# Performance work log

Hardware: AMD Instinct MI355X
Metric: run time of the kernel (lower is better)

Reference implementation:

```python
import jax, jax.numpy as jnp
import numpy as np

SQRT2 = 1.4142135623730951
MH_C = 0.8673250705840776  # (2/sqrt(3)) * pi**(-1/4), mexican-hat normalizer


def _bn(x, eps=1e-5):
    # BatchNorm (training-mode batch stats, default affine gamma=1, beta=0)
    mu = jnp.mean(x, axis=0, keepdims=True)
    var = jnp.var(x, axis=0, keepdims=True)
    return (x - mu) / jnp.sqrt(var + eps)


def setup_inputs() -> dict:
    key = jax.random.key(0)
    ks = jax.random.split(key, 10)
    N, F, E, B, OUT = 1024, 1024, 32768, 16, 10
    H = F // 2  # 512 after Haar DWT
    x = jax.random.normal(ks[0], (N, F), dtype=jnp.float32)
    edge_index = jax.random.randint(ks[1], (2, E), 0, N, dtype=jnp.int32)
    batch = jnp.sort(jax.random.randint(ks[2], (N,), 0, B, dtype=jnp.int32))
    w_att = jax.random.normal(ks[3], (2,), dtype=jnp.float32)  # Linear(2,1,bias=False)
    wk_scale = jnp.ones((H, H), dtype=jnp.float32)
    wk_trans = jax.random.normal(ks[4], (H, H), dtype=jnp.float32) * 0.1
    wk_wav_w = jax.random.normal(ks[5], (H, H), dtype=jnp.float32) * 0.05
    wk_base_w = jax.random.normal(ks[6], (H, H), dtype=jnp.float32) * 0.05
    fc1_w = jax.random.normal(ks[7], (512, F + H), dtype=jnp.float32) * 0.02
    fc1_b = jnp.zeros((512,), dtype=jnp.float32)
    fc2_w = jax.random.normal(ks[8], (OUT, 512), dtype=jnp.float32) * 0.02
    fc2_b = jnp.zeros((OUT,), dtype=jnp.float32)
    return {"x": x, "w_att": w_att, "wk_scale": wk_scale, "wk_trans": wk_trans,
            "wk_wav_w": wk_wav_w, "wk_base_w": wk_base_w, "fc1_w": fc1_w,
            "fc1_b": fc1_b, "fc2_w": fc2_w, "fc2_b": fc2_b,
            "edge_index": edge_index, "batch": batch, "num_graphs": B}


def reference(x, w_att, wk_scale, wk_trans, wk_wav_w, wk_base_w,
              fc1_w, fc1_b, fc2_w, fc2_b, edge_index, batch, num_graphs):
    N = x.shape[0]
    # --- WaveletAttention: Haar ('db1') DWT over the feature dim ---
    xe, xo = x[:, 0::2], x[:, 1::2]
    low = (xe + xo) / SQRT2            # [N, 512]
    high = (xe - xo) / SQRT2           # [N, 512]
    scores = jax.nn.sigmoid(low * w_att[0] + high * w_att[1])
    h = scores * low + (1.0 - scores) * high
    # --- GINConv aggregation (eps=0): self + sum of neighbor features ---
    src, dst = edge_index[0], edge_index[1]
    agg = h + jax.ops.segment_sum(h[src], dst, num_segments=N)  # [N, 512]
    # --- WavKAN layer 512->512 (mexican hat) ---
    xs = (agg[:, None, :] - wk_trans) / wk_scale                # [N, 512, 512]
    xs2 = xs * xs
    mh = MH_C * (1.0 - xs2) * jnp.exp(-0.5 * xs2)
    wav = jnp.einsum('noi,oi->no', mh, wk_wav_w)                # [N, 512]
    base = jax.nn.silu(agg) @ wk_base_w.T
    conv_out = _bn(wav + base)   # WavKAN-internal BatchNorm1d
    conv_out = _bn(conv_out)     # bn1 (dropout p=0 -> identity)
    # --- skip concat + bn2 ---
    z = _bn(jnp.concatenate([x, conv_out], axis=1))             # [N, 1536]
    # --- global mean pool over graphs ---
    sums = jax.ops.segment_sum(z, batch, num_segments=num_graphs)
    cnts = jax.ops.segment_sum(jnp.ones((N,), z.dtype), batch, num_segments=num_graphs)
    pooled = sums / jnp.maximum(cnts, 1.0)[:, None]             # [B, 1536]
    # --- classifier head (eval-mode dropout = identity) ---
    h1 = jax.nn.relu(pooled @ fc1_w.T + fc1_b)
    return h1 @ fc2_w.T + fc2_b
```

## Files before the change

kernel.cpp:

```cpp
#include <hip/hip_runtime.h>
#include <math.h>

#define N_NODES 1024
#define F_DIM   1024
#define H_DIM   512
#define E_EDGES 32768
#define B_GRAPHS 16
#define OUT_DIM 10
#define FH_DIM  1536
#define EPS 1e-5f
#define MH_C_D 0.8673250705840776
#define C2_D   0.72134752044448170368
#define C2_F   ((float)C2_D)
#define CSC    0.84932180028801904272f
#define WC2F   ((float)(MH_C_D / C2_D))
#define INV_SQRT2 0.70710678118654752440f
#define ECAP 128

typedef float v2f __attribute__((ext_vector_type(2)));
typedef unsigned int u32;
typedef const __attribute__((address_space(1))) u32 gu32;
typedef __attribute__((address_space(3))) u32 lu32;

#if __has_builtin(__builtin_amdgcn_exp2f)
#define EXP2NEG(x) __builtin_amdgcn_exp2f(-(x))
#else
#define EXP2NEG(x) __expf(-0.69314718055994530942f * (x))
#endif

#define PK_FMA_BB(d, a, p) \
    asm("v_pk_fma_f32 %0, %1, %2, %2 op_sel:[0,0,1] op_sel_hi:[1,0,1]" \
        : "=v"(d) : "v"(a), "v"(p))
#define PK_MUL2(d, a, b) \
    asm("v_pk_mul_f32 %0, %1, %2" : "=v"(d) : "v"(a), "v"(b))
#define PK_WZC(d, s, k) \
    asm("v_pk_mul_f32 %0, %1, %2 op_sel:[0,0] op_sel_hi:[0,1]" \
        : "=v"(d) : "v"(s), "v"(k))
#define PK_FMA_HI_ACC(acc, s, p) \
    asm("v_pk_fma_f32 %0, %1, %2, %0 op_sel:[0,1,0] op_sel_hi:[1,1,1]" \
        : "+v"(acc) : "v"(s), "v"(p))

__global__ __launch_bounds__(256) void k_hx(const int* __restrict__ src,
                                            const int* __restrict__ dst,
                                            int* __restrict__ deg,
                                            int* __restrict__ elist,
                                            const float* __restrict__ x,
                                            float* __restrict__ xsum,
                                            float* __restrict__ xsum2,
                                            const float* __restrict__ scale,
                                            const float* __restrict__ trans,
                                            const float* __restrict__ ww,
                                            const float* __restrict__ bw,
                                            float* __restrict__ pk,
                                            const float* __restrict__ watt,
                                            float* __restrict__ h) {
    const int bid = blockIdx.x;
    const int t = threadIdx.x;
    if (bid < 2048) {
        int idx = bid * 256 + t;
        float2 p = ((const float2*)x)[idx];
        float lo = (p.x + p.y) * INV_SQRT2;
        float hi = (p.x - p.y) * INV_SQRT2;
        float tt = lo * watt[0] + hi * watt[1];
        float sc = 1.0f / (1.0f + __expf(-tt));
        h[idx] = sc * lo + (1.0f - sc) * hi;
    } else if (bid < 3072) {
        int g = (bid - 2048) * 256 + t;
        float iv = 1.0f / scale[g];
        float4 p;
        p.x = iv * CSC;
        p.y = -(trans[g] * iv * CSC);
        p.z = -(ww[g] * WC2F);
        p.w = bw[g];
        ((float4*)pk)[g] = p;
    } else if (bid < 3200) {
        int e = (bid - 3072) * 256 + t;
        int d = dst[e];
        int slot = atomicAdd(&deg[d], 1);
        elist[d * ECAP + slot] = src[e];
    } else {
        const int n0 = (bid - 3200) * 16;
        float s[4] = {}, s2[4] = {};
        for (int r = 0; r < 16; ++r) {
            #pragma unroll
            for (int ch = 0; ch < 4; ++ch) {
                float v = x[(n0 + r) * F_DIM + ch * 256 + t];
                s[ch] += v; s2[ch] += v * v;
            }
        }
        #pragma unroll
        for (int ch = 0; ch < 4; ++ch) {
            unsafeAtomicAdd(&xsum[ch * 256 + t], s[ch]);
            unsafeAtomicAdd(&xsum2[ch * 256 + t], s2[ch]);
        }
    }
}

__global__ __launch_bounds__(256) void k_gather(const float* __restrict__ h,
                                                const int* __restrict__ deg,
                                                const int* __restrict__ elist,
                                                float* __restrict__ agg) {
    int d = blockIdx.x;
    int t = threadIdx.x;
    int st = d * ECAP, dg = deg[d];
    const float2* h2 = (const float2*)h;
    float2 a = h2[d * 256 + t];
    int k = 0;
    for (; k + 4 <= dg; k += 4) {
        int s0 = elist[st + k];
        int s1 = elist[st + k + 1];
        int s2 = elist[st + k + 2];
        int s3 = elist[st + k + 3];
        float2 v0 = h2[s0 * 256 + t];
        float2 v1 = h2[s1 * 256 + t];
        float2 v2 = h2[s2 * 256 + t];
        float2 v3 = h2[s3 * 256 + t];
        a.x += (v0.x + v1.x) + (v2.x + v3.x);
        a.y += (v0.y + v1.y) + (v2.y + v3.y);
    }
    for (; k < dg; ++k) {
        int s0 = elist[st + k];
        float2 v0 = h2[s0 * 256 + t];
        a.x += v0.x; a.y += v0.y;
    }
    ((float2*)agg)[d * 256 + t] = a;
}

__global__ __launch_bounds__(256) void k_transpose(const float* __restrict__ agg,
                                                   float* __restrict__ aggT,
                                                   float* __restrict__ siluT) {
    __shared__ float tile[64 * 65];
    const int t = threadIdx.x;
    const int n0 = blockIdx.x * 64;
    const int i0 = blockIdx.y * 64;
    #pragma unroll
    for (int v = 0; v < 4; ++v) {
        int flat = v * 256 + t;
        int r = flat >> 4, c4 = flat & 15;
        float4 a = *(const float4*)&agg[(n0 + r) * H_DIM + i0 + c4 * 4];
        tile[(c4 * 4 + 0) * 65 + r] = a.x;
        tile[(c4 * 4 + 1) * 65 + r] = a.y;
        tile[(c4 * 4 + 2) * 65 + r] = a.z;
        tile[(c4 * 4 + 3) * 65 + r] = a.w;
    }
    __syncthreads();
    #pragma unroll
    for (int v = 0; v < 4; ++v) {
        int flat = v * 256 + t;
        int il = flat >> 4, c4 = flat & 15;
        float4 a;
        a.x = tile[il * 65 + c4 * 4 + 0];
        a.y = tile[il * 65 + c4 * 4 + 1];
        a.z = tile[il * 65 + c4 * 4 + 2];
        a.w = tile[il * 65 + c4 * 4 + 3];
        int g = (i0 + il) * N_NODES + n0 + c4 * 4;
        *(float4*)&aggT[g] = a;
        float4 s;
        s.x = a.x / (1.0f + __expf(-a.x));
        s.y = a.y / (1.0f + __expf(-a.y));
        s.z = a.z / (1.0f + __expf(-a.z));
        s.w = a.w / (1.0f + __expf(-a.w));
        *(float4*)&siluT[g] = s;
    }
}

#define TN 128
#define TO 32
#define KI 16
#define TOP (TO + 1)
#define ZSPLIT 8
#define ZLEN (H_DIM / ZSPLIT)
#define NSTG (ZLEN / KI)
__global__ __launch_bounds__(256) void k_wavelet(const float* __restrict__ aggT,
                                                 const float* __restrict__ siluT,
                                                 const float* __restrict__ pk,
                                                 float* __restrict__ vbp) {
    __shared__ float  sA[2][KI * TN];
    __shared__ float  sS[2][KI * TN];
    __shared__ float4 sP4[2][KI * TOP];

    const int t  = threadIdx.x;
    const int n0 = blockIdx.x * TN;
    const int o0 = blockIdx.y * TO;
    const int z0 = blockIdx.z * ZLEN;
    const int na = (t & 15) * 4;
    const int ol = (t >> 4) * 2;

    const int srow = t >> 5, scol = (t & 31) * 4;
    const int po  = t >> 4;
    const int pii = t & 15;
    const float4* pk4 = (const float4*)pk;

    v2f accw[2][4] = {};
    v2f accb[2][4] = {};
    v2f kC2; kC2.x = 1.0f; kC2.y = -C2_F;

    {
        int g0 = (z0 + srow) * N_NODES + n0 + scol;
        int g1 = (z0 + 8 + srow) * N_NODES + n0 + scol;
        __builtin_amdgcn_global_load_lds((gu32*)&aggT[g0],  (lu32*)&sA[0][t * 4], 16, 0, 0);
        __builtin_amdgcn_global_load_lds((gu32*)&aggT[g1],  (lu32*)&sA[0][1024 + t * 4], 16, 0, 0);
        __builtin_amdgcn_global_load_lds((gu32*)&siluT[g0], (lu32*)&sS[0][t * 4], 16, 0, 0);
        __builtin_amdgcn_global_load_lds((gu32*)&siluT[g1], (lu32*)&sS[0][1024 + t * 4], 16, 0, 0);
        float4 r0 = pk4[(size_t)(o0 + po) * H_DIM + z0 + pii];
        float4 r1 = pk4[(size_t)(o0 + po + 16) * H_DIM + z0 + pii];
        sP4[0][pii * TOP + po]      = r0;
        sP4[0][pii * TOP + po + 16] = r1;
    }
    __syncthreads();

    for (int stg = 0; stg < NSTG; ++stg) {
        const int i0 = z0 + stg * KI;
        const int nb = (stg + 1) & 1;
        float4 r0, r1;
        if (stg + 1 < NSTG) {
            int g0 = (i0 + KI + srow) * N_NODES + n0 + scol;
            int g1 = (i0 + KI + 8 + srow) * N_NODES + n0 + scol;
            __builtin_amdgcn_global_load_lds((gu32*)&aggT[g0],
                                             (lu32*)&sA[nb][t * 4], 16, 0, 0);
            __builtin_amdgcn_global_load_lds((gu32*)&aggT[g1],
                                             (lu32*)&sA[nb][1024 + t * 4], 16, 0, 0);
            __builtin_amdgcn_global_load_lds((gu32*)&siluT[g0],
                                             (lu32*)&sS[nb][t * 4], 16, 0, 0);
            __builtin_amdgcn_global_load_lds((gu32*)&siluT[g1],
                                             (lu32*)&sS[nb][1024 + t * 4], 16, 0, 0);
            r0 = pk4[(size_t)(o0 + po) * H_DIM + i0 + KI + pii];
            r1 = pk4[(size_t)(o0 + po + 16) * H_DIM + i0 + KI + pii];
        }
        const float*  pA = sA[stg & 1];
        const float*  pS = sS[stg & 1];
        const float4* pP = sP4[stg & 1];
        #pragma unroll 4
        for (int ii = 0; ii < KI; ++ii) {
            float4 af0 = *(const float4*)&pA[ii * TN + na];
            float4 af1 = *(const float4*)&pA[ii * TN + 64 + na];
            float4 sf0 = *(const float4*)&pS[ii * TN + na];
            float4 sf1 = *(const float4*)&pS[ii * TN + 64 + na];
            v2f a01 = {af0.x, af0.y}, a23 = {af0.z, af0.w};
            v2f a45 = {af1.x, af1.y}, a67 = {af1.z, af1.w};
            v2f s01 = {sf0.x, sf0.y}, s23 = {sf0.z, sf0.w};
            v2f s45 = {sf1.x, sf1.y}, s67 = {sf1.z, sf1.w};
            #pragma unroll
            for (int oo = 0; oo < 2; ++oo) {
                float4 pq = pP[ii * TOP + ol + oo];
                v2f pxy = {pq.x, pq.y};
                v2f pzw = {pq.z, pq.w};
                v2f wzc; PK_WZC(wzc, pzw, kC2);
                v2f y0, y1, y2, y3, q0, q1, q2, q3, w0, w1, w2, w3;
                PK_FMA_BB(y0, a01, pxy); PK_FMA_BB(y1, a23, pxy);
                PK_FMA_BB(y2, a45, pxy); PK_FMA_BB(y3, a67, pxy);
                PK_MUL2(q0, y0, y0); PK_MUL2(q1, y1, y1);
                PK_MUL2(q2, y2, y2); PK_MUL2(q3, y3, y3);
                PK_FMA_BB(w0, q0, wzc); PK_FMA_BB(w1, q1, wzc);
                PK_FMA_BB(w2, q2, wzc); PK_FMA_BB(w3, q3, wzc);
                accw[oo][0].x += w0.x * EXP2NEG(q0.x);
                accw[oo][0].y += w0.y * EXP2NEG(q0.y);
                accw[oo][1].x += w1.x * EXP2NEG(q1.x);
                accw[oo][1].y += w1.y * EXP2NEG(q1.y);
                accw[oo][2].x += w2.x * EXP2NEG(q2.x);
                accw[oo][2].y += w2.y * EXP2NEG(q2.y);
                accw[oo][3].x += w3.x * EXP2NEG(q3.x);
                accw[oo][3].y += w3.y * EXP2NEG(q3.y);
                PK_FMA_HI_ACC(accb[oo][0], s01, pzw);
                PK_FMA_HI_ACC(accb[oo][1], s23, pzw);
                PK_FMA_HI_ACC(accb[oo][2], s45, pzw);
                PK_FMA_HI_ACC(accb[oo][3], s67, pzw);
            }
        }
        if (stg + 1 < NSTG) {
            sP4[nb][pii * TOP + po]      = r0;
            sP4[nb][pii * TOP + po + 16] = r1;
        }
        __syncthreads();
    }
    float* out = vbp + (size_t)blockIdx.z * (N_NODES * H_DIM);
    #pragma unroll
    for (int p = 0; p < 4; ++p) {
        int rn = n0 + ((p & 2) ? 64 : 0) + na + (p & 1) * 2;
        float2 lo, hi;
        lo.x = accw[0][p].x + accb[0][p].x;
        lo.y = accw[1][p].x + accb[1][p].x;
        hi.x = accw[0][p].y + accb[0][p].y;
        hi.y = accw[1][p].y + accb[1][p].y;
        *(float2*)&out[(size_t)rn * H_DIM + o0 + ol]       = lo;
        *(float2*)&out[(size_t)(rn + 1) * H_DIM + o0 + ol] = hi;
    }
}

__global__ __launch_bounds__(256) void k_reduce(const float* __restrict__ vbp,
                                                float* __restrict__ vb,
                                                float* __restrict__ colsum,
                                                float* __restrict__ colsum2) {
    const int b = blockIdx.x;
    const int o0 = (b & 7) * 64;
    const int n0 = (b >> 3) * 64;
    const int t = threadIdx.x;
    const int oc = o0 + (t & 63);
    const int nsub = t >> 6;
    float s = 0.f, s2 = 0.f;
    for (int r = 0; r < 16; ++r) {
        int n = n0 + r * 4 + nsub;
        size_t idx = (size_t)n * H_DIM + oc;
        float v = 0.f;
        #pragma unroll
        for (int z = 0; z < ZSPLIT; ++z) v += vbp[z * (N_NODES * H_DIM) + idx];
        vb[idx] = v;
        s += v; s2 += v * v;
    }
    __shared__ float sh1[256], sh2[256];
    sh1[t] = s; sh2[t] = s2;
    __syncthreads();
    if (t < 64) {
        s  = sh1[t] + sh1[t + 64] + sh1[t + 128] + sh1[t + 192];
        s2 = sh2[t] + sh2[t + 64] + sh2[t + 128] + sh2[t + 192];
        unsafeAtomicAdd(&colsum[o0 + t], s);
        unsafeAtomicAdd(&colsum2[o0 + t], s2);
    }
}

__global__ __launch_bounds__(256) void k_pool(const float* __restrict__ x,
                                              const float* __restrict__ vb,
                                              const int* __restrict__ batch,
                                              const float* __restrict__ colsum,
                                              const float* __restrict__ colsum2,
                                              const float* __restrict__ xsum,
                                              const float* __restrict__ xsum2,
                                              float* __restrict__ pooled) {
    const int b = blockIdx.x;
    const int ch = blockIdx.y;
    const int t = threadIdx.x;

    __shared__ int s_cnt[4];
    __shared__ int s_st;
    int c = 0;
    for (int n = t; n < N_NODES; n += 256) {
        int bb = batch[n];
        int pb = (n == 0) ? -1 : batch[n - 1];
        c += (bb == b) ? 1 : 0;
        if (bb == b && pb != b) s_st = n;
    }
    #pragma unroll
    for (int off = 32; off > 0; off >>= 1) c += __shfl_down(c, off);
    if ((t & 63) == 0) s_cnt[t >> 6] = c;
    __syncthreads();
    int cnt = s_cnt[0] + s_cnt[1] + s_cnt[2] + s_cnt[3];
    int st = (cnt > 0) ? s_st : 0;
    float ic = (cnt > 0) ? 1.0f / (float)cnt : 0.f;

    float acc = 0.f;
    if (ch < 4) {
        int col = ch * 256 + t;
        float mu  = xsum[col] * (1.0f / N_NODES);
        float var = xsum2[col] * (1.0f / N_NODES) - mu * mu;
        if (var < 0.f) var = 0.f;
        float S = 1.0f / sqrtf(var + EPS);
        const float* base = x + col;
        for (int r = 0; r < cnt; ++r) acc += base[(size_t)(st + r) * F_DIM];
        pooled[b * FH_DIM + col] = (acc * ic - mu) * S;
    } else {
        int col = (ch - 4) * 256 + t;
        float mu  = colsum[col] * (1.0f / N_NODES);
        float var = colsum2[col] * (1.0f / N_NODES) - mu * mu;
        if (var < 0.f) var = 0.f;
        float s1v = 1.0f / sqrtf(var + EPS);
        float v1  = var * s1v * s1v;
        float s2v = 1.0f / sqrtf(v1 + EPS);
        float v2  = v1 * s2v * s2v;
        float s3v = 1.0f / sqrtf(v2 + EPS);
        float S = s1v * s2v * s3v;
        const float* base = vb + col;
        for (int r = 0; r < cnt; ++r) acc += base[(size_t)(st + r) * H_DIM];
        pooled[b * FH_DIM + F_DIM + col] = (acc * ic - mu) * S;
    }
}

__global__ __launch_bounds__(256) void k_fc1(const float* __restrict__ pooled,
                                             const float* __restrict__ w,
                                             const float* __restrict__ bias,
                                             float* __restrict__ h1) {
    int wid = (blockIdx.x * 256 + threadIdx.x) >> 6;
    int lane = threadIdx.x & 63;
    int b = wid >> 9, o = wid & 511;
    const float4* pr = (const float4*)(pooled + b * FH_DIM);
    const float4* wr = (const float4*)(w + o * FH_DIM);
    float acc = 0.f;
    #pragma unroll
    for (int k = 0; k < 6; ++k) {
        float4 a = pr[k * 64 + lane];
        float4 v = wr[k * 64 + lane];
        acc += a.x * v.x + a.y * v.y + a.z * v.z + a.w * v.w;
    }
    #pragma unroll
    for (int off = 32; off > 0; off >>= 1) acc += __shfl_down(acc, off);
    if (lane == 0) h1[b * H_DIM + o] = fmaxf(acc + bias[o], 0.f);
}

__global__ __launch_bounds__(256) void k_fc2(const float* __restrict__ h1,
                                             const float* __restrict__ w,
                                             const float* __restrict__ bias,
                                             float* __restrict__ outp) {
    int wid = (blockIdx.x * 256 + threadIdx.x) >> 6;
    int lane = threadIdx.x & 63;
    if (wid >= B_GRAPHS * OUT_DIM) return;
    int b = wid / OUT_DIM, u = wid % OUT_DIM;
    const float4* hr = (const float4*)(h1 + b * H_DIM);
    const float4* wr = (const float4*)(w + u * H_DIM);
    float acc = 0.f;
    #pragma unroll
    for (int k = 0; k < 2; ++k) {
        float4 a = hr[k * 64 + lane];
        float4 v = wr[k * 64 + lane];
        acc += a.x * v.x + a.y * v.y + a.z * v.z + a.w * v.w;
    }
    #pragma unroll
    for (int off = 32; off > 0; off >>= 1) acc += __shfl_down(acc, off);
    if (lane == 0) outp[b * OUT_DIM + u] = acc + bias[u];
}

extern "C" void kernel_launch(void* const* d_in, const int* in_sizes, int n_in,
                              void* d_out, int out_size, void* d_ws, size_t ws_size,
                              hipStream_t stream) {
    const float* x       = (const float*)d_in[0];
    const float* w_att   = (const float*)d_in[1];
    const float* wk_scale= (const float*)d_in[2];
    const float* wk_trans= (const float*)d_in[3];
    const float* wk_wav  = (const float*)d_in[4];
    const float* wk_base = (const float*)d_in[5];
    const float* fc1_w   = (const float*)d_in[6];
    const float* fc1_b   = (const float*)d_in[7];
    const float* fc2_w   = (const float*)d_in[8];
    const float* fc2_b   = (const float*)d_in[9];
    const int*   eidx    = (const int*)d_in[10];
    const int*   batch   = (const int*)d_in[11];
    float* outp = (float*)d_out;

    float* ws = (float*)d_ws;
    const int NH = N_NODES * H_DIM;
    float* h      = ws;
    float* agg    = h + NH;
    float* aggT   = agg + NH;
    float* siluT  = aggT + NH;
    float* pk     = siluT + NH;
    float* vbp    = pk + 4 * (H_DIM * H_DIM);
    float* vb     = vbp + (size_t)ZSPLIT * NH;
    float* colsum = vb + NH;
    float* colsum2= colsum + 512;
    float* xsum   = colsum2 + 512;
    float* xsum2  = xsum + 1024;
    int*   deg    = (int*)(xsum2 + 1024);
    int*   elist  = deg + N_NODES;
    float* pooled = (float*)(elist + N_NODES * ECAP);
    float* h1     = pooled + B_GRAPHS * FH_DIM;

    const int* src = eidx;
    const int* dst = eidx + E_EDGES;

    hipMemsetAsync(colsum, 0, 4096 * sizeof(float), stream);
    k_hx<<<3264, 256, 0, stream>>>(src, dst, deg, elist, x, xsum, xsum2,
                                   wk_scale, wk_trans, wk_wav, wk_base, pk, w_att, h);
    k_gather<<<N_NODES, 256, 0, stream>>>(h, deg, elist, agg);
    {
        dim3 grid(N_NODES / 64, H_DIM / 64);
        k_transpose<<<grid, 256, 0, stream>>>(agg, aggT, siluT);
    }
    {
        dim3 grid(N_NODES / TN, H_DIM / TO, ZSPLIT);
        k_wavelet<<<grid, 256, 0, stream>>>(aggT, siluT, pk, vbp);
    }
    k_reduce<<<128, 256, 0, stream>>>(vbp, vb, colsum, colsum2);
    {
        dim3 grid(B_GRAPHS, 6);
        k_pool<<<grid, 256, 0, stream>>>(x, vb, batch, colsum, colsum2, xsum, xsum2, pooled);
    }
    k_fc1<<<(B_GRAPHS * H_DIM * 64) / 256, 256, 0, stream>>>(pooled, fc1_w, fc1_b, h1);
    k_fc2<<<(B_GRAPHS * OUT_DIM * 64 + 255) / 256, 256, 0, stream>>>(h1, fc2_w, fc2_b, outp);
}
```

Baseline: 185.4 us.

## Fuse neighbor gather with transpose and reuse fc1 weights across graphs

Merges the GIN neighbor-sum gather and the agg transpose/SiLU into one kernel, so the intermediate agg buffer is never written or re-read and one launch is dropped. Each block now gathers a 16-node by 64-feature tile with scalar loads, transposes it in shared memory, and writes aggT and siluT. Separately, fc1 now keeps each weight row in registers and loops over all 16 graphs, instead of reloading the row once per graph. The trade-offs are narrower scalar gather loads, each block fetching edge lists for only 16 nodes, and fewer blocks in fc1.

```diff
diff --git a/kernel.cpp b/kernel.cpp
--- a/kernel.cpp
+++ b/kernel.cpp
@@ -96,72 +96,53 @@
     }
 }
 
-__global__ __launch_bounds__(256) void k_gather(const float* __restrict__ h,
-                                                const int* __restrict__ deg,
-                                                const int* __restrict__ elist,
-                                                float* __restrict__ agg) {
-    int d = blockIdx.x;
-    int t = threadIdx.x;
-    int st = d * ECAP, dg = deg[d];
-    const float2* h2 = (const float2*)h;
-    float2 a = h2[d * 256 + t];
-    int k = 0;
-    for (; k + 4 <= dg; k += 4) {
-        int s0 = elist[st + k];
-        int s1 = elist[st + k + 1];
-        int s2 = elist[st + k + 2];
-        int s3 = elist[st + k + 3];
-        float2 v0 = h2[s0 * 256 + t];
-        float2 v1 = h2[s1 * 256 + t];
-        float2 v2 = h2[s2 * 256 + t];
-        float2 v3 = h2[s3 * 256 + t];
-        a.x += (v0.x + v1.x) + (v2.x + v3.x);
-        a.y += (v0.y + v1.y) + (v2.y + v3.y);
-    }
-    for (; k < dg; ++k) {
-        int s0 = elist[st + k];
-        float2 v0 = h2[s0 * 256 + t];
-        a.x += v0.x; a.y += v0.y;
-    }
-    ((float2*)agg)[d * 256 + t] = a;
-}
-
-__global__ __launch_bounds__(256) void k_transpose(const float* __restrict__ agg,
-                                                   float* __restrict__ aggT,
-                                                   float* __restrict__ siluT) {
-    __shared__ float tile[64 * 65];
+#define GT_NT 16
+#define GT_IT 64
+__global__ __launch_bounds__(256) void k_gt(const float* __restrict__ h,
+                                            const int* __restrict__ deg,
+                                            const int* __restrict__ elist,
+                                            float* __restrict__ aggT,
+                                            float* __restrict__ siluT) {
+    __shared__ float tile[GT_IT][GT_NT + 1];
     const int t = threadIdx.x;
-    const int n0 = blockIdx.x * 64;
-    const int i0 = blockIdx.y * 64;
-    #pragma unroll
-    for (int v = 0; v < 4; ++v) {
-        int flat = v * 256 + t;
-        int r = flat >> 4, c4 = flat & 15;
-        float4 a = *(const float4*)&agg[(n0 + r) * H_DIM + i0 + c4 * 4];
-        tile[(c4 * 4 + 0) * 65 + r] = a.x;
-        tile[(c4 * 4 + 1) * 65 + r] = a.y;
-        tile[(c4 * 4 + 2) * 65 + r] = a.z;
-        tile[(c4 * 4 + 3) * 65 + r] = a.w;
+    const int n0 = blockIdx.x * GT_NT;
+    const int i0 = blockIdx.y * GT_IT;
+    const int il = t & 63;
+    const int nl = t >> 6;
+    const int ii = i0 + il;
+    #pragma unroll
+    for (int p = 0; p < GT_NT / 4; ++p) {
+        int n = n0 + p * 4 + nl;
+        const int* el = elist + n * ECAP;
+        int dg = deg[n];
+        float acc = h[(size_t)n * H_DIM + ii];
+        int k = 0;
+        for (; k + 4 <= dg; k += 4) {
+            int s0 = el[k], s1 = el[k + 1], s2 = el[k + 2], s3 = el[k + 3];
+            float v0 = h[(size_t)s0 * H_DIM + ii];
+            float v1 = h[(size_t)s1 * H_DIM + ii];
+            float v2 = h[(size_t)s2 * H_DIM + ii];
+            float v3 = h[(size_t)s3 * H_DIM + ii];
+            acc += (v0 + v1) + (v2 + v3);
+        }
+        for (; k < dg; ++k) acc += h[(size_t)el[k] * H_DIM + ii];
+        tile[il][p * 4 + nl] = acc;
     }
     __syncthreads();
-    #pragma unroll
-    for (int v = 0; v < 4; ++v) {
-        int flat = v * 256 + t;
-        int il = flat >> 4, c4 = flat & 15;
-        float4 a;
-        a.x = tile[il * 65 + c4 * 4 + 0];
-        a.y = tile[il * 65 + c4 * 4 + 1];
-        a.z = tile[il * 65 + c4 * 4 + 2];
-        a.w = tile[il * 65 + c4 * 4 + 3];
-        int g = (i0 + il) * N_NODES + n0 + c4 * 4;
-        *(float4*)&aggT[g] = a;
-        float4 s;
-        s.x = a.x / (1.0f + __expf(-a.x));
-        s.y = a.y / (1.0f + __expf(-a.y));
-        s.z = a.z / (1.0f + __expf(-a.z));
-        s.w = a.w / (1.0f + __expf(-a.w));
-        *(float4*)&siluT[g] = s;
-    }
+    const int ir = t >> 2, q = t & 3;
+    float4 a;
+    a.x = tile[ir][q * 4 + 0];
+    a.y = tile[ir][q * 4 + 1];
+    a.z = tile[ir][q * 4 + 2];
+    a.w = tile[ir][q * 4 + 3];
+    size_t g = (size_t)(i0 + ir) * N_NODES + n0 + q * 4;
+    *(float4*)&aggT[g] = a;
+    float4 s;
+    s.x = a.x / (1.0f + __expf(-a.x));
+    s.y = a.y / (1.0f + __expf(-a.y));
+    s.z = a.z / (1.0f + __expf(-a.z));
+    s.w = a.w / (1.0f + __expf(-a.w));
+    *(float4*)&siluT[g] = s;
 }
 
 #define TN 128
@@ -378,21 +359,26 @@
                                              const float* __restrict__ w,
                                              const float* __restrict__ bias,
                                              float* __restrict__ h1) {
-    int wid = (blockIdx.x * 256 + threadIdx.x) >> 6;
-    int lane = threadIdx.x & 63;
-    int b = wid >> 9, o = wid & 511;
-    const float4* pr = (const float4*)(pooled + b * FH_DIM);
+    const int t = threadIdx.x;
+    const int lane = t & 63;
+    const int o = blockIdx.x * 4 + (t >> 6);
     const float4* wr = (const float4*)(w + o * FH_DIM);
-    float acc = 0.f;
-    #pragma unroll
-    for (int k = 0; k < 6; ++k) {
-        float4 a = pr[k * 64 + lane];
-        float4 v = wr[k * 64 + lane];
-        acc += a.x * v.x + a.y * v.y + a.z * v.z + a.w * v.w;
-    }
-    #pragma unroll
-    for (int off = 32; off > 0; off >>= 1) acc += __shfl_down(acc, off);
-    if (lane == 0) h1[b * H_DIM + o] = fmaxf(acc + bias[o], 0.f);
+    float4 wv[6];
+    #pragma unroll
+    for (int k = 0; k < 6; ++k) wv[k] = wr[k * 64 + lane];
+    const float bo = bias[o];
+    for (int b = 0; b < B_GRAPHS; ++b) {
+        const float4* pr = (const float4*)(pooled + b * FH_DIM);
+        float acc = 0.f;
+        #pragma unroll
+        for (int k = 0; k < 6; ++k) {
+            float4 a = pr[k * 64 + lane];
+            acc += a.x * wv[k].x + a.y * wv[k].y + a.z * wv[k].z + a.w * wv[k].w;
+        }
+        #pragma unroll
+        for (int off = 32; off > 0; off >>= 1) acc += __shfl_down(acc, off);
+        if (lane == 0) h1[b * H_DIM + o] = fmaxf(acc + bo, 0.f);
+    }
 }
 
 __global__ __launch_bounds__(256) void k_fc2(const float* __restrict__ h1,
@@ -437,8 +423,7 @@
     float* ws = (float*)d_ws;
     const int NH = N_NODES * H_DIM;
     float* h      = ws;
-    float* agg    = h + NH;
-    float* aggT   = agg + NH;
+    float* aggT   = h + NH;
     float* siluT  = aggT + NH;
     float* pk     = siluT + NH;
     float* vbp    = pk + 4 * (H_DIM * H_DIM);
@@ -458,10 +443,9 @@
     hipMemsetAsync(colsum, 0, 4096 * sizeof(float), stream);
     k_hx<<<3264, 256, 0, stream>>>(src, dst, deg, elist, x, xsum, xsum2,
                                    wk_scale, wk_trans, wk_wav, wk_base, pk, w_att, h);
-    k_gather<<<N_NODES, 256, 0, stream>>>(h, deg, elist, agg);
     {
-        dim3 grid(N_NODES / 64, H_DIM / 64);
-        k_transpose<<<grid, 256, 0, stream>>>(agg, aggT, siluT);
+        dim3 grid(N_NODES / GT_NT, H_DIM / GT_IT);
+        k_gt<<<grid, 256, 0, stream>>>(h, deg, elist, aggT, siluT);
     }
     {
         dim3 grid(N_NODES / TN, H_DIM / TO, ZSPLIT);
@@ -472,6 +456,6 @@
         dim3 grid(B_GRAPHS, 6);
         k_pool<<<grid, 256, 0, stream>>>(x, vb, batch, colsum, colsum2, xsum, xsum2, pooled);
     }
-    k_fc1<<<(B_GRAPHS * H_DIM * 64) / 256, 256, 0, stream>>>(pooled, fc1_w, fc1_b, h1);
+    k_fc1<<<H_DIM / 4, 256, 0, stream>>>(pooled, fc1_w, fc1_b, h1);
     k_fc2<<<(B_GRAPHS * OUT_DIM * 64 + 255) / 256, 256, 0, stream>>>(h1, fc2_w, fc2_b, outp);
 }
```

Measured after the change: 202.5 us. +9.3%, slower.
